# Optimization experiments

Hardware: AMD Instinct MI355X
Metric: run time of the kernel (lower is better)

Reference implementation:

```python
import jax, jax.numpy as jnp
import numpy as np

B, L, H, NH = 32, 512, 256, 4
DH = H // NH
EPS = 1e-12


def setup_inputs() -> dict:
    key = jax.random.key(0)
    ks = jax.random.split(key, 24)
    p = lambda k, shape: 0.02 * jax.random.normal(k, shape, dtype=jnp.float32)
    return {
        "input_tensor": jax.random.normal(ks[0], (B, L, H), dtype=jnp.float32),
        # sorted positive timestamps (seconds-like scale)
        "time_seq": jnp.sort(jax.random.uniform(ks[1], (B, L), dtype=jnp.float32) * 100.0, axis=-1),
        "attention_mask": jnp.zeros((B, 1, L, L), dtype=jnp.float32),
        "item_seq_len": jnp.clip(jax.random.randint(ks[2], (B,), 0, L), 2, L),
        "Wq": p(ks[3], (H, H)), "bq": jnp.zeros((H,), jnp.float32),
        "Wk": p(ks[4], (H, H)), "bk": jnp.zeros((H,), jnp.float32),
        "Wv": p(ks[5], (H, H)), "bv": jnp.zeros((H,), jnp.float32),
        "Wd": p(ks[6], (H, H)), "bd": jnp.zeros((H,), jnp.float32),
        "ln_g": jnp.ones((H,), jnp.float32), "ln_b": jnp.zeros((H,), jnp.float32),
        "Wtq": p(ks[7], (H, H)), "btq": jnp.zeros((H,), jnp.float32),
        "tw1": p(ks[8], (L, L)), "tb1": p(ks[9], (L, L)),
        "tow1": p(ks[10], (L, L)), "tow2": p(ks[11], (L, L)), "tob": p(ks[12], (L, L)),
        "Wt": p(ks[13], (1, 2 * H)), "bt": jnp.zeros((1,), jnp.float32),
    }


def reference(input_tensor, time_seq, attention_mask, item_seq_len,
              Wq, bq, Wk, bk, Wv, bv, Wd, bd, ln_g, ln_b,
              Wtq, btq, tw1, tb1, tow1, tow2, tob, Wt, bt):
    x = input_tensor  # (B, L, H)

    def heads(t):  # (B,L,H) -> (B,NH,L,DH)
        return t.reshape(B, L, NH, DH).transpose(0, 2, 1, 3)

    q = heads(x @ Wq.T + bq)
    k = heads(x @ Wk.T + bk)
    v = heads(x @ Wv.T + bv)

    scores = jnp.einsum('bhqd,bhkd->bhqk', q, k)  # (B,NH,L,L)

    # --- time decay gate ---
    tq = x @ Wtq.T + btq                                  # (B,L,H)
    time_query_key = jnp.tanh(jnp.einsum('bqh,bkh->bqk', tq, x))  # (B,L,L)
    diff = jnp.abs(time_seq[:, :, None] - time_seq[:, None, :])   # |t_i - t_j|
    decay = jnp.tanh(jnp.log1p(diff) * tw1 + tb1)
    decay_gate = tow1 * decay + tow2 * time_query_key + tob       # (B,L,L)
    time_attn = jax.nn.sigmoid(decay_gate)[:, None, :, :]         # (B,1,L,L)

    scores = scores * time_attn / jnp.sqrt(jnp.float32(DH)) + attention_mask
    probs = jax.nn.softmax(scores, axis=-1)

    ctx = jnp.einsum('bhqk,bhkd->bhqd', probs, v)
    ctx = ctx.transpose(0, 2, 1, 3).reshape(B, L, H)

    hs = ctx @ Wd.T + bd + x
    mu = jnp.mean(hs, axis=-1, keepdims=True)
    var = jnp.var(hs, axis=-1, keepdims=True)
    hs = (hs - mu) / jnp.sqrt(var + EPS) * ln_g + ln_b   # (B,L,H)

    bidx = jnp.arange(B)
    emb1 = hs[bidx, item_seq_len - 1]  # (B,H)
    emb2 = hs[bidx, item_seq_len - 2]  # (B,H)
    pred_intervals = jnp.concatenate([emb1, emb2], axis=1) @ Wt.T + bt  # (B,1)
    return hs, pred_intervals
```

## Files before the change

### kernel.cpp

```cpp
#include <hip/hip_runtime.h>
#include <math.h>

#define Bn 32
#define Ln 512
#define Hn 256
#define NHn 4
#define DHn 64

typedef __attribute__((ext_vector_type(8))) short bf16x8;
typedef __attribute__((ext_vector_type(4))) float f32x4;
typedef unsigned int uint32;

__device__ __forceinline__ short f2b(float f) {
    union { float f; uint32 u; } v; v.f = f;
    uint32 r = (v.u + 0x7FFFu + ((v.u >> 16) & 1u)) >> 16;
    return (short)r;
}
__device__ __forceinline__ float b2f(short h) {
    union { uint32 u; float f; } v; v.u = ((uint32)(unsigned short)h) << 16;
    return v.f;
}
__device__ __forceinline__ float fast_tanh(float x) {
    float e = __expf(2.f * x);
    return 1.f - 2.f * __builtin_amdgcn_rcpf(e + 1.f);
}
__device__ __forceinline__ float fast_sigmoid(float x) {
    return __builtin_amdgcn_rcpf(1.f + __expf(-x));
}

__global__ __launch_bounds__(256) void conv_kernel(
    const float* __restrict__ x,
    const float* __restrict__ Wq, const float* __restrict__ Wk,
    const float* __restrict__ Wv, const float* __restrict__ Wtq,
    const float* __restrict__ Wd,
    short* __restrict__ xb, short* __restrict__ wb)
{
    const size_t NLH = (size_t)Bn * Ln * Hn;
    size_t i4 = ((size_t)blockIdx.x * 256 + threadIdx.x) * 4;
    if (i4 < NLH) {
        float4 v = *(const float4*)(x + i4);
        short4 o; o.x = f2b(v.x); o.y = f2b(v.y); o.z = f2b(v.z); o.w = f2b(v.w);
        *(short4*)(xb + i4) = o;
    } else {
        size_t off = i4 - NLH;
        int w = (int)(off >> 16);
        size_t wi = off & 65535;
        const float* src = (w == 0) ? Wq : (w == 1) ? Wk : (w == 2) ? Wv : (w == 3) ? Wtq : Wd;
        float4 v = *(const float4*)(src + wi);
        short4 o; o.x = f2b(v.x); o.y = f2b(v.y); o.z = f2b(v.z); o.w = f2b(v.w);
        *(short4*)(wb + off) = o;
    }
}

struct Acc { f32x4 t[4]; };

__device__ __forceinline__ void gemm_tile_64(
    const short* __restrict__ A,
    const short* __restrict__ Bm,
    int K, short* As, short* Bs, Acc& acc)
{
    const int tid = threadIdx.x;
    const int lane = tid & 63, w = tid >> 6;
    const int quad = lane >> 4, lm = lane & 15;
    const int srow = tid >> 3;
    const int slot = tid & 7;

    for (int k0 = 0; k0 < K; k0 += 64) {
        __syncthreads();
#pragma unroll
        for (int iss = 0; iss < 2; ++iss) {
            int r = srow + iss * 32;
            bf16x8 av = *(const bf16x8*)(A + (size_t)r * K + k0 + slot * 8);
            bf16x8 bv = *(const bf16x8*)(Bm + (size_t)r * K + k0 + slot * 8);
            *(bf16x8*)(As + r * 72 + slot * 8) = av;
            *(bf16x8*)(Bs + r * 72 + slot * 8) = bv;
        }
        __syncthreads();
#pragma unroll
        for (int ks = 0; ks < 2; ++ks) {
            bf16x8 a = *(const bf16x8*)(As + (w * 16 + lm) * 72 + ks * 32 + quad * 8);
#pragma unroll
            for (int kt = 0; kt < 4; ++kt) {
                bf16x8 b = *(const bf16x8*)(Bs + (kt * 16 + lm) * 72 + ks * 32 + quad * 8);
                acc.t[kt] = __builtin_amdgcn_mfma_f32_16x16x32_bf16(a, b, acc.t[kt], 0, 0, 0);
            }
        }
    }
}

__global__ __launch_bounds__(256) void proj_kernel(
    const short* __restrict__ xb, const short* __restrict__ wb,
    const float* __restrict__ bq, const float* __restrict__ bk,
    const float* __restrict__ bv, const float* __restrict__ btq,
    short* __restrict__ qb, short* __restrict__ kb,
    short* __restrict__ vb, short* __restrict__ tqb)
{
    __shared__ short As[64 * 72];
    __shared__ short Bs[4][64 * 72];
    const int ncol0 = blockIdx.x * 64;
    const int m0 = blockIdx.y * 64;
    const int tid = threadIdx.x;
    const int lane = tid & 63, w = tid >> 6;
    const int quad = lane >> 4, lm = lane & 15;
    const int srow = tid >> 3, slot = tid & 7;

    f32x4 acc[4][4];
#pragma unroll
    for (int t = 0; t < 4; ++t)
#pragma unroll
        for (int i = 0; i < 4; ++i) acc[t][i] = (f32x4){0.f, 0.f, 0.f, 0.f};

    for (int k0 = 0; k0 < Hn; k0 += 64) {
        __syncthreads();
#pragma unroll
        for (int iss = 0; iss < 2; ++iss) {
            int r = srow + iss * 32;
            bf16x8 av = *(const bf16x8*)(xb + (size_t)(m0 + r) * Hn + k0 + slot * 8);
            *(bf16x8*)(As + r * 72 + slot * 8) = av;
#pragma unroll
            for (int t = 0; t < 4; ++t) {
                bf16x8 bv2 = *(const bf16x8*)(wb + (size_t)t * 65536 + (size_t)(ncol0 + r) * Hn + k0 + slot * 8);
                *(bf16x8*)(Bs[t] + r * 72 + slot * 8) = bv2;
            }
        }
        __syncthreads();
#pragma unroll
        for (int ks = 0; ks < 2; ++ks) {
            bf16x8 a = *(const bf16x8*)(As + (w * 16 + lm) * 72 + ks * 32 + quad * 8);
#pragma unroll
            for (int t = 0; t < 4; ++t)
#pragma unroll
                for (int kt = 0; kt < 4; ++kt) {
                    bf16x8 b = *(const bf16x8*)(Bs[t] + (kt * 16 + lm) * 72 + ks * 32 + quad * 8);
                    acc[t][kt] = __builtin_amdgcn_mfma_f32_16x16x32_bf16(a, b, acc[t][kt], 0, 0, 0);
                }
        }
    }

#pragma unroll
    for (int t = 0; t < 4; ++t) {
        const float* bias = (t == 0) ? bq : (t == 1) ? bk : (t == 2) ? bv : btq;
        short* out = (t == 0) ? qb : (t == 1) ? kb : (t == 2) ? vb : tqb;
#pragma unroll
        for (int kt = 0; kt < 4; ++kt) {
            int n = ncol0 + kt * 16 + lm;
            float bs = bias[n];
#pragma unroll
            for (int r = 0; r < 4; ++r) {
                int row = m0 + w * 16 + quad * 4 + r;
                out[(size_t)row * Hn + n] = f2b(acc[t][kt][r] + bs);
            }
        }
    }
}

__global__ __launch_bounds__(256) void gate_kernel(
    const short* __restrict__ tqb, const short* __restrict__ xb,
    const float* __restrict__ tseq, const float* __restrict__ mask,
    const float* __restrict__ tw1, const float* __restrict__ tb1,
    const float* __restrict__ tow1, const float* __restrict__ tow2,
    const float* __restrict__ tob,
    uint32* __restrict__ gm)
{
    __shared__ short As[64 * 72];
    __shared__ short Bs[64 * 72];
    const int b = blockIdx.z;
    const int m0 = blockIdx.y * 64, n0 = blockIdx.x * 64;
    const short* A = tqb + ((size_t)b * Ln + m0) * Hn;
    const short* Bw = xb + ((size_t)b * Ln + n0) * Hn;

    Acc acc;
#pragma unroll
    for (int i = 0; i < 4; ++i) acc.t[i] = (f32x4){0.f, 0.f, 0.f, 0.f};
    gemm_tile_64(A, Bw, Hn, As, Bs, acc);

    const int lane = threadIdx.x & 63, w = threadIdx.x >> 6;
    const int quad = lane >> 4, lm = lane & 15;
    const float* ts = tseq + (size_t)b * Ln;
    const float* mk = mask + (size_t)b * Ln * Ln;
    uint32* gout = gm + (size_t)b * Ln * Ln;
    float ti[4];
#pragma unroll
    for (int r = 0; r < 4; ++r) ti[r] = ts[m0 + w * 16 + quad * 4 + r];
#pragma unroll
    for (int kt = 0; kt < 4; ++kt) {
        int j = n0 + kt * 16 + lm;
        float tj = ts[j];
#pragma unroll
        for (int r = 0; r < 4; ++r) {
            int i = m0 + w * 16 + quad * 4 + r;
            size_t ij = (size_t)i * Ln + j;
            float lg = __logf(1.f + fabsf(ti[r] - tj));
            float dec = fast_tanh(lg * tw1[ij] + tb1[ij]);
            float tqk = fast_tanh(acc.t[kt][r]);
            float dg = tow1[ij] * dec + tow2[ij] * tqk + tob[ij];
            float g = 0.125f * fast_sigmoid(dg);
            uint32 pk = (uint32)(unsigned short)f2b(g) |
                        ((uint32)(unsigned short)f2b(mk[ij]) << 16);
            gout[ij] = pk;
        }
    }
}

__global__ __launch_bounds__(256) void flash_mfma(
    const short* __restrict__ qb, const short* __restrict__ kb,
    const short* __restrict__ vb, const uint32* __restrict__ gm,
    short* __restrict__ ctxb)
{
    __shared__ short Ks[128 * 72];
    __shared__ short Vt[64 * 136];
    __shared__ short Ps[4 * 16 * 136];
    const int q0 = blockIdx.x * 64;
    const int h = blockIdx.y, b = blockIdx.z;
    const int tid = threadIdx.x;
    const int w = tid >> 6, lane = tid & 63;
    const int quad = lane >> 4, lm = lane & 15;

    bf16x8 qf0, qf1;
    {
        const short* qrow = qb + ((size_t)(b * Ln + q0 + w * 16 + lm)) * Hn + h * DHn;
        qf0 = *(const bf16x8*)(qrow + quad * 8);
        qf1 = *(const bf16x8*)(qrow + 32 + quad * 8);
    }

    f32x4 o[4];
#pragma unroll
    for (int i = 0; i < 4; ++i) o[i] = (f32x4){0.f, 0.f, 0.f, 0.f};
    float lpart[4] = {0.f, 0.f, 0.f, 0.f};

    const uint32* gmb = gm + (size_t)b * Ln * Ln;
    const int qrow0 = q0 + w * 16 + quad * 4;

    const int srow = tid >> 3, slot = tid & 7;
    const int kp = tid & 63;
    const short* kbase = kb + ((size_t)b * Ln) * Hn + h * DHn;
    const short* vbase = vb + ((size_t)b * Ln) * Hn + h * DHn;

    bf16x8 kr[4], va0, va1, vc0, vc1;
#pragma unroll
    for (int i = 0; i < 4; ++i)
        kr[i] = *(const bf16x8*)(kbase + (size_t)(srow + 32 * i) * Hn + slot * 8);
    va0 = *(const bf16x8*)(vbase + (size_t)(2 * kp) * Hn + w * 16);
    va1 = *(const bf16x8*)(vbase + (size_t)(2 * kp) * Hn + w * 16 + 8);
    vc0 = *(const bf16x8*)(vbase + (size_t)(2 * kp + 1) * Hn + w * 16);
    vc1 = *(const bf16x8*)(vbase + (size_t)(2 * kp + 1) * Hn + w * 16 + 8);

    for (int k0 = 0; k0 < Ln; k0 += 128) {
        __syncthreads();
#pragma unroll
        for (int i = 0; i < 4; ++i)
            *(bf16x8*)(Ks + (srow + 32 * i) * 72 + slot * 8) = kr[i];
#pragma unroll
        for (int u = 0; u < 8; ++u) {
            uint32 p0 = (uint32)(unsigned short)va0[u] | ((uint32)(unsigned short)vc0[u] << 16);
            uint32 p1 = (uint32)(unsigned short)va1[u] | ((uint32)(unsigned short)vc1[u] << 16);
            *(uint32*)&Vt[(w * 16 + u) * 136 + 2 * kp] = p0;
            *(uint32*)&Vt[(w * 16 + 8 + u) * 136 + 2 * kp] = p1;
        }
        __syncthreads();

        if (k0 + 128 < Ln) {
            const short* kn = kbase + (size_t)(k0 + 128) * Hn;
            const short* vn = vbase + (size_t)(k0 + 128) * Hn;
#pragma unroll
            for (int i = 0; i < 4; ++i)
                kr[i] = *(const bf16x8*)(kn + (size_t)(srow + 32 * i) * Hn + slot * 8);
            va0 = *(const bf16x8*)(vn + (size_t)(2 * kp) * Hn + w * 16);
            va1 = *(const bf16x8*)(vn + (size_t)(2 * kp) * Hn + w * 16 + 8);
            vc0 = *(const bf16x8*)(vn + (size_t)(2 * kp + 1) * Hn + w * 16);
            vc1 = *(const bf16x8*)(vn + (size_t)(2 * kp + 1) * Hn + w * 16 + 8);
        }

        uint32 gmr[8][4];
#pragma unroll
        for (int kt = 0; kt < 8; ++kt) {
            int col = k0 + kt * 16 + lm;
#pragma unroll
            for (int r = 0; r < 4; ++r)
                gmr[kt][r] = gmb[(size_t)(qrow0 + r) * Ln + col];
        }

        f32x4 s[8];
#pragma unroll
        for (int kt = 0; kt < 8; ++kt) {
            s[kt] = (f32x4){0.f, 0.f, 0.f, 0.f};
            bf16x8 b0 = *(const bf16x8*)(Ks + (kt * 16 + lm) * 72 + quad * 8);
            s[kt] = __builtin_amdgcn_mfma_f32_16x16x32_bf16(qf0, b0, s[kt], 0, 0, 0);
            bf16x8 b1 = *(const bf16x8*)(Ks + (kt * 16 + lm) * 72 + 32 + quad * 8);
            s[kt] = __builtin_amdgcn_mfma_f32_16x16x32_bf16(qf1, b1, s[kt], 0, 0, 0);
        }

        short* pw = Ps + w * 16 * 136;
#pragma unroll
        for (int kt = 0; kt < 8; ++kt) {
#pragma unroll
            for (int r = 0; r < 4; ++r) {
                uint32 pk2 = gmr[kt][r];
                float g = b2f((short)(pk2 & 0xFFFFu));
                float m = b2f((short)(pk2 >> 16));
                float pv = __expf(s[kt][r] * g + m);
                lpart[r] += pv;
                pw[(quad * 4 + r) * 136 + kt * 16 + lm] = f2b(pv);
            }
        }
#pragma unroll
        for (int ks = 0; ks < 4; ++ks) {
            bf16x8 pa = *(const bf16x8*)(pw + lm * 136 + ks * 32 + quad * 8);
#pragma unroll
            for (int ot = 0; ot < 4; ++ot) {
                bf16x8 vv = *(const bf16x8*)(Vt + (ot * 16 + lm) * 136 + ks * 32 + quad * 8);
                o[ot] = __builtin_amdgcn_mfma_f32_16x16x32_bf16(pa, vv, o[ot], 0, 0, 0);
            }
        }
    }

#pragma unroll
    for (int r = 0; r < 4; ++r) {
        float lv = lpart[r];
#pragma unroll
        for (int off = 1; off < 16; off <<= 1) lv += __shfl_xor(lv, off, 64);
        float inv = 1.0f / lv;
        int row = b * Ln + qrow0 + r;
#pragma unroll
        for (int ot = 0; ot < 4; ++ot) {
            int d = h * DHn + ot * 16 + lm;
            ctxb[(size_t)row * Hn + d] = f2b(o[ot][r] * inv);
        }
    }
}

__global__ __launch_bounds__(256) void outln_kernel(
    const short* __restrict__ ctxb, const short* __restrict__ wdb,
    const float* __restrict__ bd, const float* __restrict__ x,
    const float* __restrict__ lng, const float* __restrict__ lnb,
    float* __restrict__ out)
{
    const int m0 = blockIdx.x * 64;
    const int tid = threadIdx.x;
    const int w = tid >> 6, lane = tid & 63;
    const int quad = lane >> 4, lm = lane & 15;

    f32x4 acc[16];
#pragma unroll
    for (int i = 0; i < 16; ++i) acc[i] = (f32x4){0.f, 0.f, 0.f, 0.f};

    const short* arow = ctxb + (size_t)(m0 + w * 16 + lm) * Hn;
#pragma unroll
    for (int ks = 0; ks < 8; ++ks) {
        bf16x8 af = *(const bf16x8*)(arow + ks * 32 + quad * 8);
#pragma unroll
        for (int nt = 0; nt < 16; ++nt) {
            bf16x8 bf_ = *(const bf16x8*)(wdb + (size_t)(nt * 16 + lm) * Hn + ks * 32 + quad * 8);
            acc[nt] = __builtin_amdgcn_mfma_f32_16x16x32_bf16(af, bf_, acc[nt], 0, 0, 0);
        }
    }

    float s1[4] = {0.f, 0.f, 0.f, 0.f}, s2[4] = {0.f, 0.f, 0.f, 0.f};
#pragma unroll
    for (int nt = 0; nt < 16; ++nt) {
        int col = nt * 16 + lm;
        float bv = bd[col];
#pragma unroll
        for (int r = 0; r < 4; ++r) {
            int row = m0 + w * 16 + quad * 4 + r;
            float v = acc[nt][r] + bv + x[(size_t)row * Hn + col];
            acc[nt][r] = v;
            s1[r] += v; s2[r] += v * v;
        }
    }
    float muv[4], rstd[4];
#pragma unroll
    for (int r = 0; r < 4; ++r) {
        float a = s1[r], b2 = s2[r];
#pragma unroll
        for (int off = 1; off < 16; off <<= 1) {
            a += __shfl_xor(a, off, 64);
            b2 += __shfl_xor(b2, off, 64);
        }
        float mu = a * (1.f / 256.f);
        float var = b2 * (1.f / 256.f) - mu * mu;
        muv[r] = mu;
        rstd[r] = rsqrtf(var + 1e-12f);
    }
#pragma unroll
    for (int nt = 0; nt < 16; ++nt) {
        int col = nt * 16 + lm;
        float gg = lng[col], bb = lnb[col];
#pragma unroll
        for (int r = 0; r < 4; ++r) {
            int row = m0 + w * 16 + quad * 4 + r;
            out[(size_t)row * Hn + col] = (acc[nt][r] - muv[r]) * rstd[r] * gg + bb;
        }
    }
}

__global__ __launch_bounds__(256) void pred_kernel(const float* __restrict__ hs,
                                                   const int* __restrict__ lens,
                                                   const float* __restrict__ Wt,
                                                   const float* __restrict__ bt,
                                                   float* __restrict__ pred)
{
    const int b = blockIdx.x, t = threadIdx.x;
    int len = lens[b];
    float e1 = hs[((size_t)b * Ln + (len - 1)) * Hn + t];
    float e2 = hs[((size_t)b * Ln + (len - 2)) * Hn + t];
    float v = e1 * Wt[t] + e2 * Wt[Hn + t];
#pragma unroll
    for (int off = 32; off > 0; off >>= 1) v += __shfl_xor(v, off, 64);
    __shared__ float ps[4];
    if ((t & 63) == 0) ps[t >> 6] = v;
    __syncthreads();
    if (t == 0) pred[b] = ps[0] + ps[1] + ps[2] + ps[3] + bt[0];
}

extern "C" void kernel_launch(void* const* d_in, const int* in_sizes, int n_in,
                              void* d_out, int out_size, void* d_ws, size_t ws_size,
                              hipStream_t stream) {
    (void)in_sizes; (void)n_in; (void)out_size; (void)ws_size;
    const float* x    = (const float*)d_in[0];
    const float* tseq = (const float*)d_in[1];
    const float* mask = (const float*)d_in[2];
    const int*   lens = (const int*)d_in[3];
    const float* Wq = (const float*)d_in[4];  const float* bq = (const float*)d_in[5];
    const float* Wk = (const float*)d_in[6];  const float* bk = (const float*)d_in[7];
    const float* Wv = (const float*)d_in[8];  const float* bv = (const float*)d_in[9];
    const float* Wd = (const float*)d_in[10]; const float* bd = (const float*)d_in[11];
    const float* ln_g = (const float*)d_in[12]; const float* ln_b = (const float*)d_in[13];
    const float* Wtq = (const float*)d_in[14]; const float* btq = (const float*)d_in[15];
    const float* tw1 = (const float*)d_in[16]; const float* tb1 = (const float*)d_in[17];
    const float* tow1 = (const float*)d_in[18]; const float* tow2 = (const float*)d_in[19];
    const float* tob = (const float*)d_in[20];
    const float* Wt = (const float*)d_in[21]; const float* bt = (const float*)d_in[22];

    const size_t NLH = (size_t)Bn * Ln * Hn;
    const size_t NLL = (size_t)Bn * Ln * Ln;
    short* ws = (short*)d_ws;
    short* xb    = ws;
    short* wb    = xb + NLH;
    short* qb    = wb + 5 * 65536;
    short* kb    = qb + NLH;
    short* vb    = kb + NLH;
    short* tqb   = vb + NLH;
    uint32* gm   = (uint32*)(tqb + NLH);
    short* ctxb  = (short*)(gm + NLL);
    float* out   = (float*)d_out;

    dim3 blk(256);
    conv_kernel<<<dim3(4416), blk, 0, stream>>>(x, Wq, Wk, Wv, Wtq, Wd, xb, wb);
    proj_kernel<<<dim3(4, 256), blk, 0, stream>>>(xb, wb, bq, bk, bv, btq, qb, kb, vb, tqb);
    gate_kernel<<<dim3(8, 8, Bn), blk, 0, stream>>>(tqb, xb, tseq, mask, tw1, tb1, tow1, tow2, tob, gm);
    flash_mfma<<<dim3(8, NHn, Bn), blk, 0, stream>>>(qb, kb, vb, gm, ctxb);
    outln_kernel<<<dim3(256), blk, 0, stream>>>(ctxb, wb + 4 * 65536, bd, x, ln_g, ln_b, out);
    pred_kernel<<<dim3(Bn), blk, 0, stream>>>(out, lens, Wt, bt, out + NLH);
}
```

Baseline: 266.2 us.

## Fuse bf16 conversion into projection and gate GEMMs, fold prediction into LayerNorm kernel

Removes the separate conversion kernel: the projection and gate GEMMs now load fp32 x and weights directly and convert to bf16 while staging into shared memory. The stage holds half of K at a time and prefetches the next half into registers. The projection grid is split per tensor (16x256 blocks) instead of computing all four outputs per block. The pred kernel is folded into the output LayerNorm epilogue using shuffles and atomics, with a memset to zero pred. This trades extra fp32 reads of x, which are now read several times, and a duplicate conversion for fewer launches and no bf16 staging buffers.

Result: slower. 322.0 us (+21.0%).

```diff
diff --git a/kernel.cpp b/kernel.cpp
--- a/kernel.cpp
+++ b/kernel.cpp
@@ -20,6 +20,12 @@
     union { uint32 u; float f; } v; v.u = ((uint32)(unsigned short)h) << 16;
     return v.f;
 }
+__device__ __forceinline__ bf16x8 cvt8(float4 a, float4 b) {
+    bf16x8 o;
+    o[0] = f2b(a.x); o[1] = f2b(a.y); o[2] = f2b(a.z); o[3] = f2b(a.w);
+    o[4] = f2b(b.x); o[5] = f2b(b.y); o[6] = f2b(b.z); o[7] = f2b(b.w);
+    return o;
+}
 __device__ __forceinline__ float fast_tanh(float x) {
     float e = __expf(2.f * x);
     return 1.f - 2.f * __builtin_amdgcn_rcpf(e + 1.f);
@@ -28,154 +34,155 @@
     return __builtin_amdgcn_rcpf(1.f + __expf(-x));
 }
 
-__global__ __launch_bounds__(256) void conv_kernel(
+__global__ __launch_bounds__(256) void proj_kernel(
     const float* __restrict__ x,
     const float* __restrict__ Wq, const float* __restrict__ Wk,
     const float* __restrict__ Wv, const float* __restrict__ Wtq,
     const float* __restrict__ Wd,
-    short* __restrict__ xb, short* __restrict__ wb)
-{
-    const size_t NLH = (size_t)Bn * Ln * Hn;
-    size_t i4 = ((size_t)blockIdx.x * 256 + threadIdx.x) * 4;
-    if (i4 < NLH) {
-        float4 v = *(const float4*)(x + i4);
-        short4 o; o.x = f2b(v.x); o.y = f2b(v.y); o.z = f2b(v.z); o.w = f2b(v.w);
-        *(short4*)(xb + i4) = o;
-    } else {
-        size_t off = i4 - NLH;
-        int w = (int)(off >> 16);
-        size_t wi = off & 65535;
-        const float* src = (w == 0) ? Wq : (w == 1) ? Wk : (w == 2) ? Wv : (w == 3) ? Wtq : Wd;
-        float4 v = *(const float4*)(src + wi);
-        short4 o; o.x = f2b(v.x); o.y = f2b(v.y); o.z = f2b(v.z); o.w = f2b(v.w);
-        *(short4*)(wb + off) = o;
-    }
-}
-
-struct Acc { f32x4 t[4]; };
-
-__device__ __forceinline__ void gemm_tile_64(
-    const short* __restrict__ A,
-    const short* __restrict__ Bm,
-    int K, short* As, short* Bs, Acc& acc)
-{
-    const int tid = threadIdx.x;
-    const int lane = tid & 63, w = tid >> 6;
-    const int quad = lane >> 4, lm = lane & 15;
-    const int srow = tid >> 3;
-    const int slot = tid & 7;
-
-    for (int k0 = 0; k0 < K; k0 += 64) {
-        __syncthreads();
-#pragma unroll
-        for (int iss = 0; iss < 2; ++iss) {
-            int r = srow + iss * 32;
-            bf16x8 av = *(const bf16x8*)(A + (size_t)r * K + k0 + slot * 8);
-            bf16x8 bv = *(const bf16x8*)(Bm + (size_t)r * K + k0 + slot * 8);
-            *(bf16x8*)(As + r * 72 + slot * 8) = av;
-            *(bf16x8*)(Bs + r * 72 + slot * 8) = bv;
-        }
-        __syncthreads();
-#pragma unroll
-        for (int ks = 0; ks < 2; ++ks) {
-            bf16x8 a = *(const bf16x8*)(As + (w * 16 + lm) * 72 + ks * 32 + quad * 8);
-#pragma unroll
-            for (int kt = 0; kt < 4; ++kt) {
-                bf16x8 b = *(const bf16x8*)(Bs + (kt * 16 + lm) * 72 + ks * 32 + quad * 8);
-                acc.t[kt] = __builtin_amdgcn_mfma_f32_16x16x32_bf16(a, b, acc.t[kt], 0, 0, 0);
-            }
-        }
-    }
-}
-
-__global__ __launch_bounds__(256) void proj_kernel(
-    const short* __restrict__ xb, const short* __restrict__ wb,
     const float* __restrict__ bq, const float* __restrict__ bk,
     const float* __restrict__ bv, const float* __restrict__ btq,
     short* __restrict__ qb, short* __restrict__ kb,
-    short* __restrict__ vb, short* __restrict__ tqb)
+    short* __restrict__ vb, short* __restrict__ tqb,
+    short* __restrict__ wdb)
 {
-    __shared__ short As[64 * 72];
-    __shared__ short Bs[4][64 * 72];
-    const int ncol0 = blockIdx.x * 64;
+    __shared__ short As[64 * 136];
+    __shared__ short Bs[64 * 136];
+    const int tid = threadIdx.x;
+
+    if (blockIdx.y == 0) {
+        int base = blockIdx.x * 4096 + tid * 16;
+#pragma unroll
+        for (int j = 0; j < 4; ++j) {
+            float4 v = *(const float4*)(Wd + base + j * 4);
+            short4 o; o.x = f2b(v.x); o.y = f2b(v.y); o.z = f2b(v.z); o.w = f2b(v.w);
+            *(short4*)(wdb + base + j * 4) = o;
+        }
+    }
+
+    const int tensor = blockIdx.x >> 2;
+    const int ncol0 = (blockIdx.x & 3) * 64;
     const int m0 = blockIdx.y * 64;
-    const int tid = threadIdx.x;
+    const float* Wsrc = (tensor == 0) ? Wq : (tensor == 1) ? Wk : (tensor == 2) ? Wv : Wtq;
+    const float* bias = (tensor == 0) ? bq : (tensor == 1) ? bk : (tensor == 2) ? bv : btq;
+    short* out = (tensor == 0) ? qb : (tensor == 1) ? kb : (tensor == 2) ? vb : tqb;
+
     const int lane = tid & 63, w = tid >> 6;
     const int quad = lane >> 4, lm = lane & 15;
-    const int srow = tid >> 3, slot = tid & 7;
-
-    f32x4 acc[4][4];
-#pragma unroll
-    for (int t = 0; t < 4; ++t)
-#pragma unroll
-        for (int i = 0; i < 4; ++i) acc[t][i] = (f32x4){0.f, 0.f, 0.f, 0.f};
-
-    for (int k0 = 0; k0 < Hn; k0 += 64) {
-        __syncthreads();
-#pragma unroll
-        for (int iss = 0; iss < 2; ++iss) {
-            int r = srow + iss * 32;
-            bf16x8 av = *(const bf16x8*)(xb + (size_t)(m0 + r) * Hn + k0 + slot * 8);
-            *(bf16x8*)(As + r * 72 + slot * 8) = av;
-#pragma unroll
-            for (int t = 0; t < 4; ++t) {
-                bf16x8 bv2 = *(const bf16x8*)(wb + (size_t)t * 65536 + (size_t)(ncol0 + r) * Hn + k0 + slot * 8);
-                *(bf16x8*)(Bs[t] + r * 72 + slot * 8) = bv2;
-            }
-        }
-        __syncthreads();
-#pragma unroll
-        for (int ks = 0; ks < 2; ++ks) {
-            bf16x8 a = *(const bf16x8*)(As + (w * 16 + lm) * 72 + ks * 32 + quad * 8);
-#pragma unroll
-            for (int t = 0; t < 4; ++t)
-#pragma unroll
-                for (int kt = 0; kt < 4; ++kt) {
-                    bf16x8 b = *(const bf16x8*)(Bs[t] + (kt * 16 + lm) * 72 + ks * 32 + quad * 8);
-                    acc[t][kt] = __builtin_amdgcn_mfma_f32_16x16x32_bf16(a, b, acc[t][kt], 0, 0, 0);
-                }
-        }
-    }
-
-#pragma unroll
-    for (int t = 0; t < 4; ++t) {
-        const float* bias = (t == 0) ? bq : (t == 1) ? bk : (t == 2) ? bv : btq;
-        short* out = (t == 0) ? qb : (t == 1) ? kb : (t == 2) ? vb : tqb;
-#pragma unroll
-        for (int kt = 0; kt < 4; ++kt) {
-            int n = ncol0 + kt * 16 + lm;
-            float bs = bias[n];
-#pragma unroll
-            for (int r = 0; r < 4; ++r) {
-                int row = m0 + w * 16 + quad * 4 + r;
-                out[(size_t)row * Hn + n] = f2b(acc[t][kt][r] + bs);
-            }
+    const int srow = tid >> 2;
+    const int cb = (tid & 3) * 32;
+
+    f32x4 acc[4];
+#pragma unroll
+    for (int i = 0; i < 4; ++i) acc[i] = (f32x4){0.f, 0.f, 0.f, 0.f};
+
+    float4 fa[8], fb[8];
+#pragma unroll
+    for (int j = 0; j < 4; ++j) {
+        fa[2*j]   = *(const float4*)(x + (size_t)(m0 + srow) * Hn + cb + j * 8);
+        fa[2*j+1] = *(const float4*)(x + (size_t)(m0 + srow) * Hn + cb + j * 8 + 4);
+        fb[2*j]   = *(const float4*)(Wsrc + (size_t)(ncol0 + srow) * Hn + cb + j * 8);
+        fb[2*j+1] = *(const float4*)(Wsrc + (size_t)(ncol0 + srow) * Hn + cb + j * 8 + 4);
+    }
+
+    for (int it = 0; it < 2; ++it) {
+        __syncthreads();
+#pragma unroll
+        for (int j = 0; j < 4; ++j) {
+            *(bf16x8*)(As + srow * 136 + cb + j * 8) = cvt8(fa[2*j], fa[2*j+1]);
+            *(bf16x8*)(Bs + srow * 136 + cb + j * 8) = cvt8(fb[2*j], fb[2*j+1]);
+        }
+        __syncthreads();
+        if (it == 0) {
+#pragma unroll
+            for (int j = 0; j < 4; ++j) {
+                fa[2*j]   = *(const float4*)(x + (size_t)(m0 + srow) * Hn + 128 + cb + j * 8);
+                fa[2*j+1] = *(const float4*)(x + (size_t)(m0 + srow) * Hn + 128 + cb + j * 8 + 4);
+                fb[2*j]   = *(const float4*)(Wsrc + (size_t)(ncol0 + srow) * Hn + 128 + cb + j * 8);
+                fb[2*j+1] = *(const float4*)(Wsrc + (size_t)(ncol0 + srow) * Hn + 128 + cb + j * 8 + 4);
+            }
+        }
+#pragma unroll
+        for (int ks = 0; ks < 4; ++ks) {
+            bf16x8 a = *(const bf16x8*)(As + (w * 16 + lm) * 136 + ks * 32 + quad * 8);
+#pragma unroll
+            for (int kt = 0; kt < 4; ++kt) {
+                bf16x8 b = *(const bf16x8*)(Bs + (kt * 16 + lm) * 136 + ks * 32 + quad * 8);
+                acc[kt] = __builtin_amdgcn_mfma_f32_16x16x32_bf16(a, b, acc[kt], 0, 0, 0);
+            }
+        }
+    }
+
+#pragma unroll
+    for (int kt = 0; kt < 4; ++kt) {
+        int n = ncol0 + kt * 16 + lm;
+        float bs = bias[n];
+#pragma unroll
+        for (int r = 0; r < 4; ++r) {
+            int row = m0 + w * 16 + quad * 4 + r;
+            out[(size_t)row * Hn + n] = f2b(acc[kt][r] + bs);
         }
     }
 }
 
 __global__ __launch_bounds__(256) void gate_kernel(
-    const short* __restrict__ tqb, const short* __restrict__ xb,
+    const short* __restrict__ tqb, const float* __restrict__ x,
     const float* __restrict__ tseq, const float* __restrict__ mask,
     const float* __restrict__ tw1, const float* __restrict__ tb1,
     const float* __restrict__ tow1, const float* __restrict__ tow2,
     const float* __restrict__ tob,
     uint32* __restrict__ gm)
 {
-    __shared__ short As[64 * 72];
-    __shared__ short Bs[64 * 72];
+    __shared__ short As[64 * 136];
+    __shared__ short Bs[64 * 136];
     const int b = blockIdx.z;
     const int m0 = blockIdx.y * 64, n0 = blockIdx.x * 64;
-    const short* A = tqb + ((size_t)b * Ln + m0) * Hn;
-    const short* Bw = xb + ((size_t)b * Ln + n0) * Hn;
-
-    Acc acc;
-#pragma unroll
-    for (int i = 0; i < 4; ++i) acc.t[i] = (f32x4){0.f, 0.f, 0.f, 0.f};
-    gemm_tile_64(A, Bw, Hn, As, Bs, acc);
-
-    const int lane = threadIdx.x & 63, w = threadIdx.x >> 6;
+    const int tid = threadIdx.x;
+    const int lane = tid & 63, w = tid >> 6;
     const int quad = lane >> 4, lm = lane & 15;
+    const int srow = tid >> 2, cb = (tid & 3) * 32;
+
+    const short* Abase = tqb + ((size_t)b * Ln + m0) * Hn;
+    const float* Bbase = x + ((size_t)b * Ln + n0) * Hn;
+
+    f32x4 acc[4];
+#pragma unroll
+    for (int i = 0; i < 4; ++i) acc[i] = (f32x4){0.f, 0.f, 0.f, 0.f};
+
+    bf16x8 ka[4]; float4 fb[8];
+#pragma unroll
+    for (int j = 0; j < 4; ++j) {
+        ka[j]     = *(const bf16x8*)(Abase + (size_t)srow * Hn + cb + j * 8);
+        fb[2*j]   = *(const float4*)(Bbase + (size_t)srow * Hn + cb + j * 8);
+        fb[2*j+1] = *(const float4*)(Bbase + (size_t)srow * Hn + cb + j * 8 + 4);
+    }
+
+    for (int it = 0; it < 2; ++it) {
+        __syncthreads();
+#pragma unroll
+        for (int j = 0; j < 4; ++j) {
+            *(bf16x8*)(As + srow * 136 + cb + j * 8) = ka[j];
+            *(bf16x8*)(Bs + srow * 136 + cb + j * 8) = cvt8(fb[2*j], fb[2*j+1]);
+        }
+        __syncthreads();
+        if (it == 0) {
+#pragma unroll
+            for (int j = 0; j < 4; ++j) {
+                ka[j]     = *(const bf16x8*)(Abase + (size_t)srow * Hn + 128 + cb + j * 8);
+                fb[2*j]   = *(const float4*)(Bbase + (size_t)srow * Hn + 128 + cb + j * 8);
+                fb[2*j+1] = *(const float4*)(Bbase + (size_t)srow * Hn + 128 + cb + j * 8 + 4);
+            }
+        }
+#pragma unroll
+        for (int ks = 0; ks < 4; ++ks) {
+            bf16x8 a = *(const bf16x8*)(As + (w * 16 + lm) * 136 + ks * 32 + quad * 8);
+#pragma unroll
+            for (int kt = 0; kt < 4; ++kt) {
+                bf16x8 bfr = *(const bf16x8*)(Bs + (kt * 16 + lm) * 136 + ks * 32 + quad * 8);
+                acc[kt] = __builtin_amdgcn_mfma_f32_16x16x32_bf16(a, bfr, acc[kt], 0, 0, 0);
+            }
+        }
+    }
+
     const float* ts = tseq + (size_t)b * Ln;
     const float* mk = mask + (size_t)b * Ln * Ln;
     uint32* gout = gm + (size_t)b * Ln * Ln;
@@ -192,7 +199,7 @@
             size_t ij = (size_t)i * Ln + j;
             float lg = __logf(1.f + fabsf(ti[r] - tj));
             float dec = fast_tanh(lg * tw1[ij] + tb1[ij]);
-            float tqk = fast_tanh(acc.t[kt][r]);
+            float tqk = fast_tanh(acc[kt][r]);
             float dg = tow1[ij] * dec + tow2[ij] * tqk + tob[ij];
             float g = 0.125f * fast_sigmoid(dg);
             uint32 pk = (uint32)(unsigned short)f2b(g) |
@@ -333,7 +340,9 @@
     const short* __restrict__ ctxb, const short* __restrict__ wdb,
     const float* __restrict__ bd, const float* __restrict__ x,
     const float* __restrict__ lng, const float* __restrict__ lnb,
-    float* __restrict__ out)
+    const int* __restrict__ lens, const float* __restrict__ Wt,
+    const float* __restrict__ bt,
+    float* __restrict__ out, float* __restrict__ pred)
 {
     const int m0 = blockIdx.x * 64;
     const int tid = threadIdx.x;
@@ -382,35 +391,45 @@
         muv[r] = mu;
         rstd[r] = rsqrtf(var + 1e-12f);
     }
+
+    const int b0 = m0 >> 9;
+    const int m0loc = m0 & 511;
+    const int len = lens[b0];
+    const int l1 = len - 1 - m0loc, l2 = len - 2 - m0loc;
+    const bool in1 = (l1 >= 0 && l1 < 64) && (w == (l1 >> 4));
+    const bool in2 = (l2 >= 0 && l2 < 64) && (w == (l2 >> 4));
+    const int q1 = (l1 >> 2) & 3, r1 = l1 & 3;
+    const int q2 = (l2 >> 2) & 3, r2 = l2 & 3;
+    float pp1 = 0.f, pp2 = 0.f;
+
 #pragma unroll
     for (int nt = 0; nt < 16; ++nt) {
         int col = nt * 16 + lm;
         float gg = lng[col], bb = lnb[col];
+        float ov[4];
 #pragma unroll
         for (int r = 0; r < 4; ++r) {
             int row = m0 + w * 16 + quad * 4 + r;
-            out[(size_t)row * Hn + col] = (acc[nt][r] - muv[r]) * rstd[r] * gg + bb;
-        }
-    }
-}
-
-__global__ __launch_bounds__(256) void pred_kernel(const float* __restrict__ hs,
-                                                   const int* __restrict__ lens,
-                                                   const float* __restrict__ Wt,
-                                                   const float* __restrict__ bt,
-                                                   float* __restrict__ pred)
-{
-    const int b = blockIdx.x, t = threadIdx.x;
-    int len = lens[b];
-    float e1 = hs[((size_t)b * Ln + (len - 1)) * Hn + t];
-    float e2 = hs[((size_t)b * Ln + (len - 2)) * Hn + t];
-    float v = e1 * Wt[t] + e2 * Wt[Hn + t];
-#pragma unroll
-    for (int off = 32; off > 0; off >>= 1) v += __shfl_xor(v, off, 64);
-    __shared__ float ps[4];
-    if ((t & 63) == 0) ps[t >> 6] = v;
-    __syncthreads();
-    if (t == 0) pred[b] = ps[0] + ps[1] + ps[2] + ps[3] + bt[0];
+            float v = (acc[nt][r] - muv[r]) * rstd[r] * gg + bb;
+            ov[r] = v;
+            out[(size_t)row * Hn + col] = v;
+        }
+        if (in1 && quad == q1) {
+            float v = (r1 == 0) ? ov[0] : (r1 == 1) ? ov[1] : (r1 == 2) ? ov[2] : ov[3];
+            pp1 += v * Wt[col];
+        }
+        if (in2 && quad == q2) {
+            float v = (r2 == 0) ? ov[0] : (r2 == 1) ? ov[1] : (r2 == 2) ? ov[2] : ov[3];
+            pp2 += v * Wt[Hn + col];
+        }
+    }
+#pragma unroll
+    for (int off = 1; off < 16; off <<= 1) {
+        pp1 += __shfl_xor(pp1, off, 64);
+        pp2 += __shfl_xor(pp2, off, 64);
+    }
+    if (in1 && quad == q1 && lm == 0) atomicAdd(&pred[b0], pp1 + bt[0]);
+    if (in2 && quad == q2 && lm == 0) atomicAdd(&pred[b0], pp2);
 }
 
 extern "C" void kernel_launch(void* const* d_in, const int* in_sizes, int n_in,
@@ -435,21 +454,21 @@
     const size_t NLH = (size_t)Bn * Ln * Hn;
     const size_t NLL = (size_t)Bn * Ln * Ln;
     short* ws = (short*)d_ws;
-    short* xb    = ws;
-    short* wb    = xb + NLH;
-    short* qb    = wb + 5 * 65536;
+    short* qb    = ws;
     short* kb    = qb + NLH;
     short* vb    = kb + NLH;
     short* tqb   = vb + NLH;
     uint32* gm   = (uint32*)(tqb + NLH);
     short* ctxb  = (short*)(gm + NLL);
+    short* wdb   = ctxb + NLH;
     float* out   = (float*)d_out;
+    float* pred  = out + NLH;
 
     dim3 blk(256);
-    conv_kernel<<<dim3(4416), blk, 0, stream>>>(x, Wq, Wk, Wv, Wtq, Wd, xb, wb);
-    proj_kernel<<<dim3(4, 256), blk, 0, stream>>>(xb, wb, bq, bk, bv, btq, qb, kb, vb, tqb);
-    gate_kernel<<<dim3(8, 8, Bn), blk, 0, stream>>>(tqb, xb, tseq, mask, tw1, tb1, tow1, tow2, tob, gm);
+    hipMemsetAsync(pred, 0, Bn * sizeof(float), stream);
+    proj_kernel<<<dim3(16, 256), blk, 0, stream>>>(x, Wq, Wk, Wv, Wtq, Wd,
+                                                   bq, bk, bv, btq, qb, kb, vb, tqb, wdb);
+    gate_kernel<<<dim3(8, 8, Bn), blk, 0, stream>>>(tqb, x, tseq, mask, tw1, tb1, tow1, tow2, tob, gm);
     flash_mfma<<<dim3(8, NHn, Bn), blk, 0, stream>>>(qb, kb, vb, gm, ctxb);
-    outln_kernel<<<dim3(256), blk, 0, stream>>>(ctxb, wb + 4 * 65536, bd, x, ln_g, ln_b, out);
-    pred_kernel<<<dim3(Bn), blk, 0, stream>>>(out, lens, Wt, bt, out + NLH);
-}
+    outln_kernel<<<dim3(256), blk, 0, stream>>>(ctxb, wdb, bd, x, ln_g, ln_b, lens, Wt, bt, out, pred);
+}
```
